# Optimization experiments

Measured on AMD Instinct MI355X. Metric: run time of the kernel, lower is better.

The kernel has to match this reference:

```python
import jax, jax.numpy as jnp
import numpy as np

B, T, D = 8, 4096, 256
K = 8192  # codebook_size


def setup_inputs() -> dict:
    key = jax.random.key(0)
    k1, k2 = jax.random.split(key)
    h = jax.random.normal(k1, (B, T, D), dtype=jnp.float32)
    # nn.init.uniform_(codebook.weight, -1.0, 1.0)
    codebook = jax.random.uniform(k2, (K, D), dtype=jnp.float32, minval=-1.0, maxval=1.0)
    return {"h": h, "codebook": codebook}


def reference(h, codebook):
    b, t, d = h.shape
    flat = h.reshape(-1, d)                              # [N, D]
    x2 = jnp.sum(flat * flat, axis=1, keepdims=True)     # [N, 1]
    c2 = jnp.sum(codebook * codebook, axis=1)[None, :]   # [1, K]
    xc = flat @ codebook.T                               # [N, K]
    dist = x2 + c2 - 2.0 * xc                            # [N, K]
    idx_flat = jnp.argmin(dist, axis=1)                  # [N] int
    q_flat = codebook[idx_flat]                          # gather [N, D]
    q = q_flat.reshape(b, t, d)
    idx = idx_flat.reshape(b, t)
    # straight-through estimator
    q_ste = h + jax.lax.stop_gradient(q - h)
    return q_ste, idx
```

## Files before the change

### kernel.cpp

```cpp
#include <hip/hip_runtime.h>

typedef short short8 __attribute__((ext_vector_type(8)));
typedef float f32x4 __attribute__((ext_vector_type(4)));

#define DIMS   256
#define KCODES 8192
#define NTOK   32768
#define BM     64
#define BN     64
#define NTILES 128
#define MARGIN 0.75f
#define CAP    3072

__device__ __forceinline__ unsigned short f2bf(float f) {
    unsigned u = __builtin_bit_cast(unsigned, f);
    unsigned r = (u + 0x7FFFu + ((u >> 16) & 1u)) >> 16;
    return (unsigned short)r;
}
__device__ __forceinline__ unsigned fenc(float f) {
    unsigned u = __builtin_bit_cast(unsigned, f);
    return ((int)u >= 0) ? (u | 0x80000000u) : ~u;
}
__device__ __forceinline__ void gload_lds16(const void* g, void* l) {
    __builtin_amdgcn_global_load_lds(
        (const __attribute__((address_space(1))) unsigned*)g,
        (__attribute__((address_space(3))) unsigned*)l, 16, 0, 0);
}

__global__ __launch_bounds__(256) void prep_kernel(const float* __restrict__ cb,
                                                   float* __restrict__ c2,
                                                   unsigned short* __restrict__ cbbf,
                                                   int do_conv) {
    int row  = blockIdx.x * 4 + (threadIdx.x >> 6);
    int lane = threadIdx.x & 63;
    float4 v = *(const float4*)(cb + (size_t)row * DIMS + (size_t)lane * 4);
    if (do_conv) {
        ushort4 s;
        s.x = f2bf(v.x); s.y = f2bf(v.y); s.z = f2bf(v.z); s.w = f2bf(v.w);
        *(ushort4*)(cbbf + (size_t)row * DIMS + (size_t)lane * 4) = s;
    }
    float s = v.x * v.x + v.y * v.y + v.z * v.z + v.w * v.w;
#pragma unroll
    for (int off = 32; off > 0; off >>= 1) s += __shfl_down(s, off);
    if (lane == 0) c2[row] = s;
}

template <bool WSBF>
__global__ __launch_bounds__(512, 4) void vq_main(const float* __restrict__ h,
                                                  const float* __restrict__ cb,
                                                  const unsigned short* __restrict__ cbbf,
                                                  const float* __restrict__ c2g,
                                                  float* __restrict__ out_q,
                                                  float* __restrict__ out_idx) {
    __shared__ __align__(16) unsigned short Bs[2][BN * DIMS];
    __shared__ unsigned mrun[BM];
    __shared__ unsigned list[CAP];
    __shared__ int cnt;

    const int tid  = threadIdx.x;
    const int lane = tid & 63;
    const int wave = tid >> 6;
    const int l15  = lane & 15;
    const int quad = lane >> 4;
    const int wm   = wave >> 2;
    const int wn   = wave & 3;
    const int tokBase = blockIdx.x * BM;

    if (tid < BM) mrun[tid] = 0x7F7FFFFFu;
    if (tid == 0) cnt = 0;

    const int srow0 = tid >> 5;
    const int scol  = (tid & 31) ^ (srow0 & 7);
    const int srcoff = srow0 * (DIMS * 2) + scol * 16;
    short8 g[4];

    auto stage = [&](int t, int buf) {
        if constexpr (WSBF) {
            const char* base = (const char*)cbbf + (size_t)t * (BN * DIMS * 2) + srcoff;
            unsigned short* l0 = &Bs[buf][wave * 512];
#pragma unroll
            for (int n = 0; n < 4; n++)
                gload_lds16(base + n * 8192, l0 + n * 4096);
        } else {
#pragma unroll
            for (int n = 0; n < 4; n++) {
                const size_t off = (size_t)(t * BN + srow0 + n * 16) * DIMS + (tid & 31) * 8;
                float4 v0 = *(const float4*)(cb + off);
                float4 v1 = *(const float4*)(cb + off + 4);
                short8 s;
                s[0] = f2bf(v0.x); s[1] = f2bf(v0.y); s[2] = f2bf(v0.z); s[3] = f2bf(v0.w);
                s[4] = f2bf(v1.x); s[5] = f2bf(v1.y); s[6] = f2bf(v1.z); s[7] = f2bf(v1.w);
                g[n] = s;
            }
        }
    };
    auto stage_write_fb = [&](int buf) {
#pragma unroll
        for (int n = 0; n < 4; n++)
            *(short8*)&Bs[buf][(srow0 + n * 16) * DIMS + scol * 8] = g[n];
    };

    stage(0, 0);

    short8 afr[2][8];
#pragma unroll
    for (int i = 0; i < 2; i++) {
        const float* base = h + (size_t)(tokBase + wm * 32 + i * 16 + l15) * DIMS + quad * 8;
#pragma unroll
        for (int kk = 0; kk < 8; kk++) {
            float4 v0 = *(const float4*)(base + kk * 32);
            float4 v1 = *(const float4*)(base + kk * 32 + 4);
            short8 s;
            s[0] = f2bf(v0.x); s[1] = f2bf(v0.y); s[2] = f2bf(v0.z); s[3] = f2bf(v0.w);
            s[4] = f2bf(v1.x); s[5] = f2bf(v1.y); s[6] = f2bf(v1.z); s[7] = f2bf(v1.w);
            afr[i][kk] = s;
        }
    }
    if constexpr (!WSBF) stage_write_fb(0);

    const int bswz = l15 & 7;
    const int bq   = (quad ^ (bswz & 3)) << 3;
    const int bx4  = (bswz & 4) << 3;

#pragma unroll 1
    for (int it = 0; it <= NTILES; ++it) {
        const int t = (it == NTILES) ? 0 : it;
        __syncthreads();
        const int cur = it & 1;
        if (it < NTILES) stage((it + 1 == NTILES) ? 0 : it + 1, cur ^ 1);

        const bool haveThr = (it > 0);
        float thr0 = 0.f, thr1 = 0.f;
        if (haveThr) {
            thr0 = __builtin_bit_cast(float, mrun[wm * 32 + l15]) + MARGIN;
            thr1 = __builtin_bit_cast(float, mrun[wm * 32 + 16 + l15]) + MARGIN;
        }
        const int cbase = t * BN + wn * 16;
        const float4 cc = *(const float4*)(c2g + cbase + quad * 4);

        const unsigned short* bp = &Bs[cur][(wn * 16 + l15) * DIMS + bq];

        f32x4 acc[2][2];
        acc[0][0] = (f32x4){0,0,0,0}; acc[0][1] = (f32x4){0,0,0,0};
        acc[1][0] = (f32x4){0,0,0,0}; acc[1][1] = (f32x4){0,0,0,0};

        __builtin_amdgcn_s_setprio(1);
#pragma unroll
        for (int kk = 0; kk < 4; kk++) {
            short8 b0 = *(const short8*)(bp + ((kk * 32) ^ bx4));
            short8 b1 = *(const short8*)(bp + (((kk + 4) * 32) ^ bx4));
            acc[0][0] = __builtin_amdgcn_mfma_f32_16x16x32_bf16(b0, afr[0][kk],     acc[0][0], 0, 0, 0);
            acc[1][0] = __builtin_amdgcn_mfma_f32_16x16x32_bf16(b0, afr[1][kk],     acc[1][0], 0, 0, 0);
            acc[0][1] = __builtin_amdgcn_mfma_f32_16x16x32_bf16(b1, afr[0][kk + 4], acc[0][1], 0, 0, 0);
            acc[1][1] = __builtin_amdgcn_mfma_f32_16x16x32_bf16(b1, afr[1][kk + 4], acc[1][1], 0, 0, 0);
        }
        __builtin_amdgcn_s_setprio(0);

        if constexpr (!WSBF) { if (it < NTILES) stage_write_fb(cur ^ 1); }

        const int code00 = cbase + quad * 4;
#pragma unroll
        for (int i = 0; i < 2; i++) {
            const int tok = wm * 32 + i * 16 + l15;
            const float th = i ? thr1 : thr0;
            float s0 = fmaf(-2.f, acc[i][0][0], fmaf(-2.f, acc[i][1][0], cc.x));
            float s1 = fmaf(-2.f, acc[i][0][1], fmaf(-2.f, acc[i][1][1], cc.y));
            float s2 = fmaf(-2.f, acc[i][0][2], fmaf(-2.f, acc[i][1][2], cc.z));
            float s3 = fmaf(-2.f, acc[i][0][3], fmaf(-2.f, acc[i][1][3], cc.w));
            float vm = fminf(fminf(s0, s1), fminf(s2, s3));
            if (haveThr) {
                const unsigned tk = (unsigned)(tok << 13);
                if (s0 <= th) { int p = atomicAdd(&cnt, 1); if (p < CAP) list[p] = tk | (unsigned)(code00 + 0); }
                if (s1 <= th) { int p = atomicAdd(&cnt, 1); if (p < CAP) list[p] = tk | (unsigned)(code00 + 1); }
                if (s2 <= th) { int p = atomicAdd(&cnt, 1); if (p < CAP) list[p] = tk | (unsigned)(code00 + 2); }
                if (s3 <= th) { int p = atomicAdd(&cnt, 1); if (p < CAP) list[p] = tk | (unsigned)(code00 + 3); }
            }
            if (it < NTILES) {
                vm = fminf(vm, __shfl_xor(vm, 16));
                vm = fminf(vm, __shfl_xor(vm, 32));
                if (quad == 0) atomicMin(&mrun[tok], __builtin_bit_cast(unsigned, vm));
            }
        }
    }
    __syncthreads();

    unsigned long long* best64 = (unsigned long long*)&Bs[0][0];
    if (tid < BM) best64[tid] = ~0ULL;
    __syncthreads();

    int n = cnt; if (n > CAP) n = CAP;
    for (int p = wave; p < n; p += 8) {
        unsigned e = list[p];
        int tok = (int)(e >> 13), code = (int)(e & 8191);
        float4 hv = *(const float4*)(h + (size_t)(tokBase + tok) * DIMS + lane * 4);
        float4 cv = *(const float4*)(cb + (size_t)code * DIMS + lane * 4);
        float d = hv.x * cv.x + hv.y * cv.y + hv.z * cv.z + hv.w * cv.w;
#pragma unroll
        for (int m = 1; m < 64; m <<= 1) d += __shfl_xor(d, m);
        float s = c2g[code] - 2.f * d;
        if (lane == 0)
            atomicMin(&best64[tok], ((unsigned long long)fenc(s) << 32) | (unsigned)code);
    }
    __syncthreads();

    if (tid < BM)
        out_idx[tokBase + tid] = (float)(unsigned)(best64[tid] & 0xFFFFFFFFULL);
#pragma unroll
    for (int e = tid; e < BM * (DIMS / 4); e += 512) {
        int r = e >> 6, c4 = e & 63;
        int idx = (int)(unsigned)(best64[r] & 0xFFFFFFFFULL);
        float4 v = *(const float4*)(cb + (size_t)idx * DIMS + c4 * 4);
        *(float4*)(out_q + (size_t)(tokBase + r) * DIMS + c4 * 4) = v;
    }
}

extern "C" void kernel_launch(void* const* d_in, const int* in_sizes, int n_in,
                              void* d_out, int out_size, void* d_ws, size_t ws_size,
                              hipStream_t stream) {
    const float* h  = (const float*)d_in[0];
    const float* cb = (const float*)d_in[1];
    float* out_q   = (float*)d_out;
    float* out_idx = (float*)d_out + (size_t)NTOK * DIMS;

    float* c2 = (float*)d_ws;
    unsigned short* cbbf = (unsigned short*)((char*)d_ws + 32768);
    const size_t needed = 32768 + (size_t)KCODES * DIMS * 2;
    const int wsbf = (ws_size >= needed) ? 1 : 0;

    prep_kernel<<<KCODES / 4, 256, 0, stream>>>(cb, c2, cbbf, wsbf);
    if (wsbf)
        vq_main<true><<<NTOK / BM, 512, 0, stream>>>(h, cb, cbbf, c2, out_q, out_idx);
    else
        vq_main<false><<<NTOK / BM, 512, 0, stream>>>(h, cb, (const unsigned short*)nullptr, c2, out_q, out_idx);
}
```

Before: 354.8 us.

## Pre-swizzle bf16 codebook into MFMA fragment layout and load B directly to registers

The prep kernel now writes the bf16 codebook in MFMA fragment order, so each wave reads its B fragments straight from global memory into registers with coalesced 16-byte loads. This removes the LDS double buffer, the async global-to-LDS staging and the per-tile __syncthreads. LDS use drops sharply and the freed space doubles the candidate-list capacity, but each wave now reads codebook tiles independently from L2 with no LDS sharing. Load latency is now covered only by issuing the next tile's loads during the current tile's epilogue.

```diff
diff --git a/kernel.cpp b/kernel.cpp
--- a/kernel.cpp
+++ b/kernel.cpp
@@ -10,7 +10,7 @@
 #define BN     64
 #define NTILES 128
 #define MARGIN 0.75f
-#define CAP    3072
+#define CAP    6144
 
 __device__ __forceinline__ unsigned short f2bf(float f) {
     unsigned u = __builtin_bit_cast(unsigned, f);
@@ -21,28 +21,33 @@
     unsigned u = __builtin_bit_cast(unsigned, f);
     return ((int)u >= 0) ? (u | 0x80000000u) : ~u;
 }
-__device__ __forceinline__ void gload_lds16(const void* g, void* l) {
-    __builtin_amdgcn_global_load_lds(
-        (const __attribute__((address_space(1))) unsigned*)g,
-        (__attribute__((address_space(3))) unsigned*)l, 16, 0, 0);
-}
 
 __global__ __launch_bounds__(256) void prep_kernel(const float* __restrict__ cb,
                                                    float* __restrict__ c2,
                                                    unsigned short* __restrict__ cbbf,
                                                    int do_conv) {
-    int row  = blockIdx.x * 4 + (threadIdx.x >> 6);
-    int lane = threadIdx.x & 63;
-    float4 v = *(const float4*)(cb + (size_t)row * DIMS + (size_t)lane * 4);
-    if (do_conv) {
-        ushort4 s;
-        s.x = f2bf(v.x); s.y = f2bf(v.y); s.z = f2bf(v.z); s.w = f2bf(v.w);
-        *(ushort4*)(cbbf + (size_t)row * DIMS + (size_t)lane * 4) = s;
-    }
-    float s = v.x * v.x + v.y * v.y + v.z * v.z + v.w * v.w;
-#pragma unroll
-    for (int off = 32; off > 0; off >>= 1) s += __shfl_down(s, off);
-    if (lane == 0) c2[row] = s;
+    const int g    = blockIdx.x * 4 + (threadIdx.x >> 6);
+    const int lane = threadIdx.x & 63;
+    const int l15  = lane & 15;
+    const int quad = lane >> 4;
+    const float* rp = cb + (size_t)(g * 16 + l15) * DIMS + quad * 8;
+    float ss = 0.f;
+#pragma unroll
+    for (int kk = 0; kk < 8; kk++) {
+        float4 v0 = *(const float4*)(rp + kk * 32);
+        float4 v1 = *(const float4*)(rp + kk * 32 + 4);
+        ss += v0.x * v0.x + v0.y * v0.y + v0.z * v0.z + v0.w * v0.w
+            + v1.x * v1.x + v1.y * v1.y + v1.z * v1.z + v1.w * v1.w;
+        if (do_conv) {
+            short8 s;
+            s[0] = f2bf(v0.x); s[1] = f2bf(v0.y); s[2] = f2bf(v0.z); s[3] = f2bf(v0.w);
+            s[4] = f2bf(v1.x); s[5] = f2bf(v1.y); s[6] = f2bf(v1.z); s[7] = f2bf(v1.w);
+            *(short8*)(cbbf + (size_t)g * 4096 + kk * 512 + lane * 8) = s;
+        }
+    }
+    ss += __shfl_xor(ss, 16);
+    ss += __shfl_xor(ss, 32);
+    if (quad == 0) c2[g * 16 + l15] = ss;
 }
 
 template <bool WSBF>
@@ -52,9 +57,9 @@
                                                   const float* __restrict__ c2g,
                                                   float* __restrict__ out_q,
                                                   float* __restrict__ out_idx) {
-    __shared__ __align__(16) unsigned short Bs[2][BN * DIMS];
     __shared__ unsigned mrun[BM];
     __shared__ unsigned list[CAP];
+    __shared__ unsigned long long best64[BM];
     __shared__ int cnt;
 
     const int tid  = threadIdx.x;
@@ -69,39 +74,6 @@
     if (tid < BM) mrun[tid] = 0x7F7FFFFFu;
     if (tid == 0) cnt = 0;
 
-    const int srow0 = tid >> 5;
-    const int scol  = (tid & 31) ^ (srow0 & 7);
-    const int srcoff = srow0 * (DIMS * 2) + scol * 16;
-    short8 g[4];
-
-    auto stage = [&](int t, int buf) {
-        if constexpr (WSBF) {
-            const char* base = (const char*)cbbf + (size_t)t * (BN * DIMS * 2) + srcoff;
-            unsigned short* l0 = &Bs[buf][wave * 512];
-#pragma unroll
-            for (int n = 0; n < 4; n++)
-                gload_lds16(base + n * 8192, l0 + n * 4096);
-        } else {
-#pragma unroll
-            for (int n = 0; n < 4; n++) {
-                const size_t off = (size_t)(t * BN + srow0 + n * 16) * DIMS + (tid & 31) * 8;
-                float4 v0 = *(const float4*)(cb + off);
-                float4 v1 = *(const float4*)(cb + off + 4);
-                short8 s;
-                s[0] = f2bf(v0.x); s[1] = f2bf(v0.y); s[2] = f2bf(v0.z); s[3] = f2bf(v0.w);
-                s[4] = f2bf(v1.x); s[5] = f2bf(v1.y); s[6] = f2bf(v1.z); s[7] = f2bf(v1.w);
-                g[n] = s;
-            }
-        }
-    };
-    auto stage_write_fb = [&](int buf) {
-#pragma unroll
-        for (int n = 0; n < 4; n++)
-            *(short8*)&Bs[buf][(srow0 + n * 16) * DIMS + scol * 8] = g[n];
-    };
-
-    stage(0, 0);
-
     short8 afr[2][8];
 #pragma unroll
     for (int i = 0; i < 2; i++) {
@@ -116,19 +88,35 @@
             afr[i][kk] = s;
         }
     }
-    if constexpr (!WSBF) stage_write_fb(0);
-
-    const int bswz = l15 & 7;
-    const int bq   = (quad ^ (bswz & 3)) << 3;
-    const int bx4  = (bswz & 4) << 3;
+
+    __syncthreads();
+
+    short8 bfr[8];
+    const char* fb = (const char*)cbbf + (size_t)wn * 8192 + (size_t)lane * 16;
+    auto loadB = [&](int t) {
+        if constexpr (WSBF) {
+            const char* p = fb + (size_t)t * 32768;
+#pragma unroll
+            for (int n = 0; n < 8; n++)
+                bfr[n] = *(const short8*)(p + n * 1024);
+        } else {
+            const float* rp = cb + (size_t)(t * BN + wn * 16 + l15) * DIMS + quad * 8;
+#pragma unroll
+            for (int kk = 0; kk < 8; kk++) {
+                float4 v0 = *(const float4*)(rp + kk * 32);
+                float4 v1 = *(const float4*)(rp + kk * 32 + 4);
+                short8 s;
+                s[0] = f2bf(v0.x); s[1] = f2bf(v0.y); s[2] = f2bf(v0.z); s[3] = f2bf(v0.w);
+                s[4] = f2bf(v1.x); s[5] = f2bf(v1.y); s[6] = f2bf(v1.z); s[7] = f2bf(v1.w);
+                bfr[kk] = s;
+            }
+        }
+    };
+    loadB(0);
 
 #pragma unroll 1
     for (int it = 0; it <= NTILES; ++it) {
         const int t = (it == NTILES) ? 0 : it;
-        __syncthreads();
-        const int cur = it & 1;
-        if (it < NTILES) stage((it + 1 == NTILES) ? 0 : it + 1, cur ^ 1);
-
         const bool haveThr = (it > 0);
         float thr0 = 0.f, thr1 = 0.f;
         if (haveThr) {
@@ -138,8 +126,6 @@
         const int cbase = t * BN + wn * 16;
         const float4 cc = *(const float4*)(c2g + cbase + quad * 4);
 
-        const unsigned short* bp = &Bs[cur][(wn * 16 + l15) * DIMS + bq];
-
         f32x4 acc[2][2];
         acc[0][0] = (f32x4){0,0,0,0}; acc[0][1] = (f32x4){0,0,0,0};
         acc[1][0] = (f32x4){0,0,0,0}; acc[1][1] = (f32x4){0,0,0,0};
@@ -147,8 +133,8 @@
         __builtin_amdgcn_s_setprio(1);
 #pragma unroll
         for (int kk = 0; kk < 4; kk++) {
-            short8 b0 = *(const short8*)(bp + ((kk * 32) ^ bx4));
-            short8 b1 = *(const short8*)(bp + (((kk + 4) * 32) ^ bx4));
+            short8 b0 = bfr[kk];
+            short8 b1 = bfr[kk + 4];
             acc[0][0] = __builtin_amdgcn_mfma_f32_16x16x32_bf16(b0, afr[0][kk],     acc[0][0], 0, 0, 0);
             acc[1][0] = __builtin_amdgcn_mfma_f32_16x16x32_bf16(b0, afr[1][kk],     acc[1][0], 0, 0, 0);
             acc[0][1] = __builtin_amdgcn_mfma_f32_16x16x32_bf16(b1, afr[0][kk + 4], acc[0][1], 0, 0, 0);
@@ -156,7 +142,7 @@
         }
         __builtin_amdgcn_s_setprio(0);
 
-        if constexpr (!WSBF) { if (it < NTILES) stage_write_fb(cur ^ 1); }
+        if (it < NTILES) loadB((it + 1 == NTILES) ? 0 : it + 1);
 
         const int code00 = cbase + quad * 4;
 #pragma unroll
@@ -184,7 +170,6 @@
     }
     __syncthreads();
 
-    unsigned long long* best64 = (unsigned long long*)&Bs[0][0];
     if (tid < BM) best64[tid] = ~0ULL;
     __syncthreads();
 
@@ -227,7 +212,7 @@
     const size_t needed = 32768 + (size_t)KCODES * DIMS * 2;
     const int wsbf = (ws_size >= needed) ? 1 : 0;
 
-    prep_kernel<<<KCODES / 4, 256, 0, stream>>>(cb, c2, cbbf, wsbf);
+    prep_kernel<<<KCODES / 16 / 4, 256, 0, stream>>>(cb, c2, cbbf, wsbf);
     if (wsbf)
         vq_main<true><<<NTOK / BM, 512, 0, stream>>>(h, cb, cbbf, c2, out_q, out_idx);
     else
```

New measurement: 409.3 us. 15.4% more time.
